# Kernel tuning notes

Measured on AMD Instinct MI355X. Metric: run time of the kernel, lower is better.

Reference implementation:

```python
import jax, jax.numpy as jnp
import numpy as np

K = 1024          # num_embeddings
D = 256           # embedding_dim
COMMITMENT = 0.25


def setup_inputs() -> dict:
    key = jax.random.key(0)
    k1, k2, k3 = jax.random.split(key, 3)
    return {
        "inputs": jax.random.normal(k1, (64, 2048, D), dtype=jnp.float32),
        "pre_w": jax.random.normal(k2, (D, D), dtype=jnp.float32) / jnp.sqrt(jnp.float32(D)),
        "pre_b": jnp.zeros((D,), dtype=jnp.float32),
        "emb": jax.random.uniform(k3, (K, D), dtype=jnp.float32, minval=-1.0, maxval=1.0),
    }


def reference(inputs, pre_w, pre_b, emb):
    # flatten to tokens [N, D] and apply pre_linear
    flat = inputs.reshape(-1, D)
    f = flat @ pre_w.T + pre_b                       # [N, D]
    # squared euclidean distances to codebook: ||f||^2 + ||e||^2 - 2 f e^T
    distances = (jnp.sum(f * f, axis=1, keepdims=True)
                 + jnp.sum(emb * emb, axis=1)
                 - 2.0 * (f @ emb.T))                # [N, K]
    idx = jnp.argmin(distances, axis=1)              # [N]
    encodings = jax.nn.one_hot(idx, K, dtype=inputs.dtype)  # [N, K]
    # quantized = encodings @ emb  ==  gather rows of codebook
    quantized = emb[idx].reshape(inputs.shape)       # [B, S, D]
    # commitment loss (quantized detached)
    e_latent_loss = jnp.mean((jax.lax.stop_gradient(quantized) - inputs) ** 2)
    loss = COMMITMENT * e_latent_loss
    # straight-through estimator
    quantized_st = inputs + jax.lax.stop_gradient(quantized - inputs)
    avg_probs = jnp.mean(encodings, axis=0)          # [K]
    perplexity = jnp.exp(-jnp.sum(avg_probs * jnp.log(avg_probs + 1e-10)))
    return loss, quantized_st, perplexity, encodings
```

## Files before the change

### kernel.cpp

```cpp
#include <hip/hip_runtime.h>
#include <math.h>

#define NTOK 131072
#define DDIM 256
#define KCB  1024

static constexpr size_t O_Q = 1;
static constexpr size_t O_P = 1 + (size_t)NTOK * DDIM;
static constexpr size_t O_E = O_P + 1;
static constexpr size_t SCRATCH_F_OFF = O_E + 2;
static constexpr size_t SCRATCH_FHI   = SCRATCH_F_OFF + (size_t)NTOK * DDIM;
static constexpr size_t SCRATCH_FLO   = SCRATCH_FHI + (size_t)NTOK * DDIM / 2;
static constexpr size_t SCRATCH_EHI   = SCRATCH_FLO + (size_t)NTOK * DDIM / 2;
static constexpr size_t SCRATCH_ELO   = SCRATCH_EHI + (size_t)KCB * DDIM / 2;
static constexpr size_t SCRATCH_FLG   = SCRATCH_ELO + (size_t)KCB * DDIM / 2;

static constexpr size_t WS_IDX   = 0;
static constexpr size_t WS_EN    = (size_t)NTOK * 4;
static constexpr size_t WS_CNT   = WS_EN + (size_t)KCB * 4;
static constexpr size_t WS_ACC   = WS_CNT + (size_t)KCB * 4;
static constexpr size_t WS_FLAGN = WS_ACC + 8;

#define TS 128
#define KC 32
#define LDSROW 36

#define EPS_GAP 0.0625f

typedef short bf16x8 __attribute__((ext_vector_type(8)));
typedef float f32x4  __attribute__((ext_vector_type(4)));
typedef unsigned short us4v __attribute__((ext_vector_type(4)));

__device__ __forceinline__ unsigned short f2bf(float x) {
    unsigned u = __float_as_uint(x);
    return (unsigned short)((u + 0x7FFFu + ((u >> 16) & 1u)) >> 16);
}
__device__ __forceinline__ float bf2f(unsigned short h) {
    return __uint_as_float(((unsigned)h) << 16);
}

__global__ __launch_bounds__(64) void k_enorm(const float* __restrict__ emb,
                                              float* __restrict__ enorm,
                                              unsigned short* __restrict__ ehi,
                                              unsigned short* __restrict__ elo) {
    int k = blockIdx.x;
    float4 v = reinterpret_cast<const float4*>(emb)[(size_t)k * 64 + threadIdx.x];
    float s = v.x * v.x + v.y * v.y + v.z * v.z + v.w * v.w;

    float xs[4] = {v.x, v.y, v.z, v.w};
    us4v hv, lv;
#pragma unroll
    for (int i = 0; i < 4; ++i) {
        unsigned short h = f2bf(xs[i]);
        hv[i] = h;
        lv[i] = f2bf(xs[i] - bf2f(h));
    }
    *reinterpret_cast<us4v*>(ehi + (size_t)k * DDIM + threadIdx.x * 4) = hv;
    *reinterpret_cast<us4v*>(elo + (size_t)k * DDIM + threadIdx.x * 4) = lv;

    for (int off = 32; off >= 1; off >>= 1) s += __shfl_down(s, off, 64);
    if (threadIdx.x == 0) enorm[k] = s;
}

__device__ __forceinline__ void tile_fma(const float* __restrict__ sA,
                                         const float* __restrict__ sB,
                                         int tx, int ty,
                                         float acc[8][8]) {
#pragma unroll 1
    for (int is = 0; is < 8; ++is) {
        float4 bv[8];
#pragma unroll
        for (int c = 0; c < 8; ++c)
            bv[c] = *reinterpret_cast<const float4*>(&sB[(tx + 16 * c) * LDSROW + is * 4]);
#pragma unroll
        for (int j = 0; j < 8; ++j) {
            float4 a = *reinterpret_cast<const float4*>(&sA[(ty + 16 * j) * LDSROW + is * 4]);
#pragma unroll
            for (int c = 0; c < 8; ++c)
                acc[j][c] += a.x * bv[c].x + a.y * bv[c].y + a.z * bv[c].z + a.w * bv[c].w;
        }
    }
}

__device__ __forceinline__ void stage_tiles(const float4* __restrict__ a4, size_t a_row0,
                                            const float4* __restrict__ b4, size_t b_row0,
                                            int kc, int tid,
                                            float* __restrict__ sA, float* __restrict__ sB) {
#pragma unroll
    for (int l0 = 0; l0 < 4; ++l0) {
        int l = l0 * 256 + tid;
        int row = l >> 3, i4 = l & 7;
        *reinterpret_cast<float4*>(&sA[row * LDSROW + i4 * 4]) =
            a4[(a_row0 + row) * 64 + kc * 8 + i4];
        *reinterpret_cast<float4*>(&sB[row * LDSROW + i4 * 4]) =
            b4[(b_row0 + row) * 64 + kc * 8 + i4];
    }
}

__global__ __launch_bounds__(256, 2) void k_gemm1(const float* __restrict__ x,
                                                  const float* __restrict__ w,
                                                  const float* __restrict__ b,
                                                  float* __restrict__ f,
                                                  unsigned short* __restrict__ fhi,
                                                  unsigned short* __restrict__ flo) {
    __shared__ float sA[TS * LDSROW];
    __shared__ float sB[TS * LDSROW];
    const int tid = threadIdx.x;
    const int tx = tid & 15, ty = tid >> 4;
    const int tb = blockIdx.x * TS;
    const int db = blockIdx.y * TS;

    float acc[8][8];
#pragma unroll
    for (int j = 0; j < 8; ++j)
#pragma unroll
        for (int c = 0; c < 8; ++c) acc[j][c] = 0.f;

    const float4* x4 = reinterpret_cast<const float4*>(x);
    const float4* w4 = reinterpret_cast<const float4*>(w);

#pragma unroll 1
    for (int kc = 0; kc < DDIM / KC; ++kc) {
        __syncthreads();
        stage_tiles(x4, tb, w4, db, kc, tid, sA, sB);
        __syncthreads();
        tile_fma(sA, sB, tx, ty, acc);
    }

    float bias[8];
#pragma unroll
    for (int c = 0; c < 8; ++c) bias[c] = b[db + tx + 16 * c];
#pragma unroll
    for (int j = 0; j < 8; ++j) {
        size_t rowo = (size_t)(tb + ty + 16 * j) * DDIM + db;
#pragma unroll
        for (int c = 0; c < 8; ++c) {
            float v = acc[j][c] + bias[c];
            int col = tx + 16 * c;
            f[rowo + col] = v;
            unsigned short h = f2bf(v);
            fhi[rowo + col] = h;
            flo[rowo + col] = f2bf(v - bf2f(h));
        }
    }
}

__global__ __launch_bounds__(256, 2) void k_argmin_mfma(
        const unsigned short* __restrict__ fhi, const unsigned short* __restrict__ flo,
        const unsigned short* __restrict__ ehi, const unsigned short* __restrict__ elo,
        const float* __restrict__ enorm,
        int* __restrict__ idx, int* __restrict__ flaglist, unsigned* __restrict__ flagn) {
    __shared__ bf16x8 sB[1024];
    const int tid  = threadIdx.x;
    const int lane = tid & 63;
    const int wv   = tid >> 6;
    const int row  = lane & 15;
    const int kg   = lane >> 4;
    const int tok0 = blockIdx.x * 128 + wv * 32;

    bf16x8 ah[2][8], al[2][8];
#pragma unroll
    for (int m = 0; m < 2; ++m)
#pragma unroll
        for (int kk = 0; kk < 8; ++kk) {
            size_t off = (size_t)(tok0 + m * 16 + row) * DDIM + kk * 32 + kg * 8;
            ah[m][kk] = *reinterpret_cast<const bf16x8*>(fhi + off);
            al[m][kk] = *reinterpret_cast<const bf16x8*>(flo + off);
        }

    float bd1[2][4], bd2[2][4];
    int   bk1[2][4];
#pragma unroll
    for (int m = 0; m < 2; ++m)
#pragma unroll
        for (int r = 0; r < 4; ++r) { bd1[m][r] = 3.4e38f; bd2[m][r] = 3.4e38f; bk1[m][r] = 0; }

    const int sxr = row & 7;

#pragma unroll 1
    for (int nt = 0; nt < KCB / 16; ++nt) {
        bf16x8 st[4];
#pragma unroll
        for (int i = 0; i < 4; ++i) {
            int c = i * 256 + tid;
            int code = (c >> 5) & 15, ch = c & 31;
            const unsigned short* src = (c < 512) ? ehi : elo;
            st[i] = *reinterpret_cast<const bf16x8*>(src + (size_t)(nt * 16 + code) * DDIM + ch * 8);
        }
        __syncthreads();
#pragma unroll
        for (int i = 0; i < 4; ++i) {
            int c = i * 256 + tid;
            int code = (c >> 5) & 15, ch = c & 31;
            sB[((c < 512) ? 0 : 512) + code * 32 + (ch ^ (code & 7))] = st[i];
        }
        __syncthreads();

        f32x4 acc0a = {0.f, 0.f, 0.f, 0.f}, acc0b = {0.f, 0.f, 0.f, 0.f};
        f32x4 acc1a = {0.f, 0.f, 0.f, 0.f}, acc1b = {0.f, 0.f, 0.f, 0.f};
#pragma unroll
        for (int kk = 0; kk < 8; ++kk) {
            int slot = row * 32 + (((kk * 4) + kg) ^ sxr);
            bf16x8 bh = sB[slot];
            bf16x8 bl = sB[512 + slot];
            acc0a = __builtin_amdgcn_mfma_f32_16x16x32_bf16(ah[0][kk], bh, acc0a, 0, 0, 0);
            acc1a = __builtin_amdgcn_mfma_f32_16x16x32_bf16(ah[1][kk], bh, acc1a, 0, 0, 0);
            acc0b = __builtin_amdgcn_mfma_f32_16x16x32_bf16(al[0][kk], bh, acc0b, 0, 0, 0);
            acc1b = __builtin_amdgcn_mfma_f32_16x16x32_bf16(al[1][kk], bh, acc1b, 0, 0, 0);
            acc0b = __builtin_amdgcn_mfma_f32_16x16x32_bf16(ah[0][kk], bl, acc0b, 0, 0, 0);
            acc1b = __builtin_amdgcn_mfma_f32_16x16x32_bf16(ah[1][kk], bl, acc1b, 0, 0, 0);
        }

        int code = nt * 16 + row;
        float en = enorm[code];
#pragma unroll
        for (int r = 0; r < 4; ++r) {
            float d0 = en - 2.f * (acc0a[r] + acc0b[r]);
            float d1 = en - 2.f * (acc1a[r] + acc1b[r]);
            if (d0 < bd1[0][r]) { bd2[0][r] = bd1[0][r]; bd1[0][r] = d0; bk1[0][r] = code; }
            else if (d0 < bd2[0][r]) bd2[0][r] = d0;
            if (d1 < bd1[1][r]) { bd2[1][r] = bd1[1][r]; bd1[1][r] = d1; bk1[1][r] = code; }
            else if (d1 < bd2[1][r]) bd2[1][r] = d1;
        }
    }

#pragma unroll
    for (int m = 0; m < 2; ++m)
#pragma unroll
        for (int r = 0; r < 4; ++r) {
            float v1 = bd1[m][r], v2 = bd2[m][r];
            int k1 = bk1[m][r];
#pragma unroll
            for (int msk = 1; msk < 16; msk <<= 1) {
                float o1 = __shfl_xor(v1, msk, 16);
                float o2 = __shfl_xor(v2, msk, 16);
                int   ok = __shfl_xor(k1, msk, 16);
                if (o1 < v1 || (o1 == v1 && ok < k1)) { v2 = fminf(v1, o2); v1 = o1; k1 = ok; }
                else                                  { v2 = fminf(v2, o1); }
            }
            if (row == 0) {
                int t = tok0 + m * 16 + kg * 4 + r;
                idx[t] = k1;
                if (v2 - v1 < EPS_GAP) {
                    unsigned p = atomicAdd(flagn, 1u);
                    flaglist[p] = t;
                }
            }
        }
}

__global__ __launch_bounds__(256) void k_rescore(const float* __restrict__ f,
                                                 const float* __restrict__ emb,
                                                 const float* __restrict__ enorm,
                                                 const int* __restrict__ flaglist,
                                                 const unsigned* __restrict__ flagn,
                                                 int* __restrict__ idx) {
    __shared__ float sf[DDIM];
    __shared__ float swd[4];
    __shared__ int   swk[4];
    const int tid = threadIdx.x;
    const unsigned n = *flagn;
    for (unsigned ii = blockIdx.x; ii < n; ii += gridDim.x) {
        const int t = flaglist[ii];
        __syncthreads();
        sf[tid] = f[(size_t)t * DDIM + tid];
        __syncthreads();
        float bd = 3.4e38f;
        int   bk = 0;
#pragma unroll 1
        for (int j = 0; j < 4; ++j) {
            int k = j * 256 + tid;
            const float4* er = reinterpret_cast<const float4*>(emb + (size_t)k * DDIM);
            float dot = 0.f;
#pragma unroll 8
            for (int q = 0; q < 64; ++q) {
                float4 ev = er[q];
                float4 fv = *reinterpret_cast<const float4*>(&sf[q * 4]);
                dot += ev.x * fv.x + ev.y * fv.y + ev.z * fv.z + ev.w * fv.w;
            }
            float d = enorm[k] - 2.f * dot;
            if (d < bd || (d == bd && k < bk)) { bd = d; bk = k; }
        }
        for (int m = 1; m < 64; m <<= 1) {
            float od = __shfl_xor(bd, m, 64);
            int   ok = __shfl_xor(bk, m, 64);
            if (od < bd || (od == bd && ok < bk)) { bd = od; bk = ok; }
        }
        if ((tid & 63) == 0) { swd[tid >> 6] = bd; swk[tid >> 6] = bk; }
        __syncthreads();
        if (tid == 0) {
            for (int w2 = 1; w2 < 4; ++w2)
                if (swd[w2] < bd || (swd[w2] == bd && swk[w2] < bk)) { bd = swd[w2]; bk = swk[w2]; }
            idx[t] = bk;
        }
    }
}

__global__ __launch_bounds__(256) void k_epilogue(const float* __restrict__ x,
                                                  const float* __restrict__ emb,
                                                  const int* __restrict__ idx,
                                                  float* __restrict__ out,
                                                  unsigned* __restrict__ counts,
                                                  double* __restrict__ lossacc) {
    const int tid = threadIdx.x;
    const int tb = blockIdx.x * 64;
    const float4* x4 = reinterpret_cast<const float4*>(x);
    const float4* e4 = reinterpret_cast<const float4*>(emb);
    float local = 0.f;
#pragma unroll
    for (int it = 0; it < 16; ++it) {
        int l = it * 256 + tid;
        int tok = l >> 6, q = l & 63;
        int t = tb + tok;
        int id = idx[t];
        if (q == 0) atomicAdd(&counts[id], 1u);
        float4 xv = x4[(size_t)t * 64 + q];
        float4 ev = e4[(size_t)id * 64 + q];
        size_t o = O_Q + (size_t)t * DDIM + (size_t)q * 4;
        out[o] = ev.x; out[o + 1] = ev.y; out[o + 2] = ev.z; out[o + 3] = ev.w;
        float dx = ev.x - xv.x, dy = ev.y - xv.y, dz = ev.z - xv.z, dw = ev.w - xv.w;
        local += dx * dx + dy * dy + dz * dz + dw * dw;
    }
    for (int off = 32; off >= 1; off >>= 1) local += __shfl_down(local, off, 64);
    __shared__ float wsum[4];
    if ((tid & 63) == 0) wsum[tid >> 6] = local;
    __syncthreads();
    if (tid == 0)
        atomicAdd(lossacc, (double)(wsum[0] + wsum[1] + wsum[2] + wsum[3]));
}

__global__ __launch_bounds__(256) void k_scatter(const int* __restrict__ idx,
                                                 float* __restrict__ out) {
    int t = blockIdx.x * 256 + threadIdx.x;
    out[O_E + (size_t)t * KCB + idx[t]] = 1.0f;
}

__global__ __launch_bounds__(1024) void k_final(const unsigned* __restrict__ counts,
                                                const double* __restrict__ lossacc,
                                                float* __restrict__ out) {
    int tid = threadIdx.x;
    double p = (double)counts[tid] / (double)NTOK;
    double term = p * log(p + 1e-10);
    for (int off = 32; off >= 1; off >>= 1) term += __shfl_down(term, off, 64);
    __shared__ double sw[16];
    if ((tid & 63) == 0) sw[tid >> 6] = term;
    __syncthreads();
    if (tid == 0) {
        double s = 0.0;
        for (int i = 0; i < 16; ++i) s += sw[i];
        out[O_P] = (float)exp(-s);
        out[0]   = (float)(0.25 * lossacc[0] / ((double)NTOK * (double)DDIM));
    }
}

extern "C" void kernel_launch(void* const* d_in, const int* in_sizes, int n_in,
                              void* d_out, int out_size, void* d_ws, size_t ws_size,
                              hipStream_t stream) {
    const float* x   = (const float*)d_in[0];
    const float* w   = (const float*)d_in[1];
    const float* b   = (const float*)d_in[2];
    const float* emb = (const float*)d_in[3];
    float* out = (float*)d_out;

    int*      idx    = (int*)((char*)d_ws + WS_IDX);
    float*    enorm  = (float*)((char*)d_ws + WS_EN);
    unsigned* counts = (unsigned*)((char*)d_ws + WS_CNT);
    double*   acc    = (double*)((char*)d_ws + WS_ACC);
    unsigned* flagn  = (unsigned*)((char*)d_ws + WS_FLAGN);

    float*          scratchF = out + SCRATCH_F_OFF;
    unsigned short* fhi      = (unsigned short*)(out + SCRATCH_FHI);
    unsigned short* flo      = (unsigned short*)(out + SCRATCH_FLO);
    unsigned short* ehi      = (unsigned short*)(out + SCRATCH_EHI);
    unsigned short* elo      = (unsigned short*)(out + SCRATCH_ELO);
    int*            flaglist = (int*)(out + SCRATCH_FLG);

    hipMemsetAsync((char*)d_ws + WS_CNT, 0, (size_t)KCB * 4 + 16, stream);

    k_enorm      <<<KCB,                        64,  0, stream>>>(emb, enorm, ehi, elo);
    k_gemm1      <<<dim3(NTOK / TS, DDIM / TS), 256, 0, stream>>>(x, w, b, scratchF, fhi, flo);
    k_argmin_mfma<<<NTOK / 128,                 256, 0, stream>>>(fhi, flo, ehi, elo, enorm,
                                                                 idx, flaglist, flagn);
    k_rescore    <<<128,                        256, 0, stream>>>(scratchF, emb, enorm,
                                                                 flaglist, flagn, idx);
    k_epilogue   <<<NTOK / 64,                  256, 0, stream>>>(x, emb, idx, out, counts, acc);

    hipMemsetAsync(out + O_E, 0, (size_t)NTOK * KCB * 4, stream);
    k_scatter<<<NTOK / 256, 256, 0, stream>>>(idx, out);
    k_final  <<<1,          1024, 0, stream>>>(counts, acc, out);
}
```

Before: 1.677 ms.

## Drop fp32 feature scratch, fuse one-hot write into epilogue, prefetch GEMM tiles

Removes the fp32 f scratch buffer: gemm1 writes only bf16 hi/lo splits, and rescore recomputes f for flagged tokens from x, w and bias. The memset and scatter for the one-hot encodings are replaced by a single pass in the epilogue that writes each full row directly. The next tiles are register-prefetched in gemm1 and in the argmin codebook staging so global loads overlap compute. These changes cut DRAM traffic and kernel launches, at the cost of extra register pressure and redundant matvec work in rescore.

```diff
diff --git a/kernel.cpp b/kernel.cpp
--- a/kernel.cpp
+++ b/kernel.cpp
@@ -8,12 +8,11 @@
 static constexpr size_t O_Q = 1;
 static constexpr size_t O_P = 1 + (size_t)NTOK * DDIM;
 static constexpr size_t O_E = O_P + 1;
-static constexpr size_t SCRATCH_F_OFF = O_E + 2;
-static constexpr size_t SCRATCH_FHI   = SCRATCH_F_OFF + (size_t)NTOK * DDIM;
-static constexpr size_t SCRATCH_FLO   = SCRATCH_FHI + (size_t)NTOK * DDIM / 2;
-static constexpr size_t SCRATCH_EHI   = SCRATCH_FLO + (size_t)NTOK * DDIM / 2;
-static constexpr size_t SCRATCH_ELO   = SCRATCH_EHI + (size_t)KCB * DDIM / 2;
-static constexpr size_t SCRATCH_FLG   = SCRATCH_ELO + (size_t)KCB * DDIM / 2;
+static constexpr size_t SCRATCH_FHI = O_E + 2;
+static constexpr size_t SCRATCH_FLO = SCRATCH_FHI + (size_t)NTOK * DDIM / 2;
+static constexpr size_t SCRATCH_EHI = SCRATCH_FLO + (size_t)NTOK * DDIM / 2;
+static constexpr size_t SCRATCH_ELO = SCRATCH_EHI + (size_t)KCB * DDIM / 2;
+static constexpr size_t SCRATCH_FLG = SCRATCH_ELO + (size_t)KCB * DDIM / 2;
 
 static constexpr size_t WS_IDX   = 0;
 static constexpr size_t WS_EN    = (size_t)NTOK * 4;
@@ -82,25 +81,9 @@
     }
 }
 
-__device__ __forceinline__ void stage_tiles(const float4* __restrict__ a4, size_t a_row0,
-                                            const float4* __restrict__ b4, size_t b_row0,
-                                            int kc, int tid,
-                                            float* __restrict__ sA, float* __restrict__ sB) {
-#pragma unroll
-    for (int l0 = 0; l0 < 4; ++l0) {
-        int l = l0 * 256 + tid;
-        int row = l >> 3, i4 = l & 7;
-        *reinterpret_cast<float4*>(&sA[row * LDSROW + i4 * 4]) =
-            a4[(a_row0 + row) * 64 + kc * 8 + i4];
-        *reinterpret_cast<float4*>(&sB[row * LDSROW + i4 * 4]) =
-            b4[(b_row0 + row) * 64 + kc * 8 + i4];
-    }
-}
-
 __global__ __launch_bounds__(256, 2) void k_gemm1(const float* __restrict__ x,
                                                   const float* __restrict__ w,
                                                   const float* __restrict__ b,
-                                                  float* __restrict__ f,
                                                   unsigned short* __restrict__ fhi,
                                                   unsigned short* __restrict__ flo) {
     __shared__ float sA[TS * LDSROW];
@@ -119,11 +102,33 @@
     const float4* x4 = reinterpret_cast<const float4*>(x);
     const float4* w4 = reinterpret_cast<const float4*>(w);
 
+    const int pr = tid >> 3, pi = tid & 7;
+    float4 pa[4], pb[4];
+#pragma unroll
+    for (int l0 = 0; l0 < 4; ++l0) {
+        int row = l0 * 32 + pr;
+        pa[l0] = x4[(size_t)(tb + row) * 64 + pi];
+        pb[l0] = w4[(size_t)(db + row) * 64 + pi];
+    }
+
 #pragma unroll 1
     for (int kc = 0; kc < DDIM / KC; ++kc) {
         __syncthreads();
-        stage_tiles(x4, tb, w4, db, kc, tid, sA, sB);
-        __syncthreads();
+#pragma unroll
+        for (int l0 = 0; l0 < 4; ++l0) {
+            int row = l0 * 32 + pr;
+            *reinterpret_cast<float4*>(&sA[row * LDSROW + pi * 4]) = pa[l0];
+            *reinterpret_cast<float4*>(&sB[row * LDSROW + pi * 4]) = pb[l0];
+        }
+        __syncthreads();
+        if (kc < DDIM / KC - 1) {
+#pragma unroll
+            for (int l0 = 0; l0 < 4; ++l0) {
+                int row = l0 * 32 + pr;
+                pa[l0] = x4[(size_t)(tb + row) * 64 + (kc + 1) * 8 + pi];
+                pb[l0] = w4[(size_t)(db + row) * 64 + (kc + 1) * 8 + pi];
+            }
+        }
         tile_fma(sA, sB, tx, ty, acc);
     }
 
@@ -137,7 +142,6 @@
         for (int c = 0; c < 8; ++c) {
             float v = acc[j][c] + bias[c];
             int col = tx + 16 * c;
-            f[rowo + col] = v;
             unsigned short h = f2bf(v);
             fhi[rowo + col] = h;
             flo[rowo + col] = f2bf(v - bf2f(h));
@@ -176,17 +180,20 @@
         for (int r = 0; r < 4; ++r) { bd1[m][r] = 3.4e38f; bd2[m][r] = 3.4e38f; bk1[m][r] = 0; }
 
     const int sxr = row & 7;
+    const int pcode = (tid >> 5) & 15, pch = tid & 31;
+    const bool plo = tid >= 512 / 1;
+
+    bf16x8 st[4];
+#pragma unroll
+    for (int i = 0; i < 4; ++i) {
+        int c = i * 256 + tid;
+        int code = (c >> 5) & 15, ch = c & 31;
+        const unsigned short* src = (c < 512) ? ehi : elo;
+        st[i] = *reinterpret_cast<const bf16x8*>(src + (size_t)code * DDIM + ch * 8);
+    }
 
 #pragma unroll 1
     for (int nt = 0; nt < KCB / 16; ++nt) {
-        bf16x8 st[4];
-#pragma unroll
-        for (int i = 0; i < 4; ++i) {
-            int c = i * 256 + tid;
-            int code = (c >> 5) & 15, ch = c & 31;
-            const unsigned short* src = (c < 512) ? ehi : elo;
-            st[i] = *reinterpret_cast<const bf16x8*>(src + (size_t)(nt * 16 + code) * DDIM + ch * 8);
-        }
         __syncthreads();
 #pragma unroll
         for (int i = 0; i < 4; ++i) {
@@ -195,6 +202,16 @@
             sB[((c < 512) ? 0 : 512) + code * 32 + (ch ^ (code & 7))] = st[i];
         }
         __syncthreads();
+        if (nt < KCB / 16 - 1) {
+#pragma unroll
+            for (int i = 0; i < 4; ++i) {
+                int c = i * 256 + tid;
+                int code = (c >> 5) & 15, ch = c & 31;
+                const unsigned short* src = (c < 512) ? ehi : elo;
+                st[i] = *reinterpret_cast<const bf16x8*>(
+                    src + (size_t)((nt + 1) * 16 + code) * DDIM + ch * 8);
+            }
+        }
 
         f32x4 acc0a = {0.f, 0.f, 0.f, 0.f}, acc0b = {0.f, 0.f, 0.f, 0.f};
         f32x4 acc1a = {0.f, 0.f, 0.f, 0.f}, acc1b = {0.f, 0.f, 0.f, 0.f};
@@ -249,12 +266,15 @@
         }
 }
 
-__global__ __launch_bounds__(256) void k_rescore(const float* __restrict__ f,
+__global__ __launch_bounds__(256) void k_rescore(const float* __restrict__ x,
+                                                 const float* __restrict__ w,
+                                                 const float* __restrict__ bias,
                                                  const float* __restrict__ emb,
                                                  const float* __restrict__ enorm,
                                                  const int* __restrict__ flaglist,
                                                  const unsigned* __restrict__ flagn,
                                                  int* __restrict__ idx) {
+    __shared__ float sx[DDIM];
     __shared__ float sf[DDIM];
     __shared__ float swd[4];
     __shared__ int   swk[4];
@@ -263,7 +283,17 @@
     for (unsigned ii = blockIdx.x; ii < n; ii += gridDim.x) {
         const int t = flaglist[ii];
         __syncthreads();
-        sf[tid] = f[(size_t)t * DDIM + tid];
+        sx[tid] = x[(size_t)t * DDIM + tid];
+        __syncthreads();
+        const float4* wr = reinterpret_cast<const float4*>(w + (size_t)tid * DDIM);
+        float fd = bias[tid];
+#pragma unroll 8
+        for (int q = 0; q < 64; ++q) {
+            float4 wv = wr[q];
+            float4 xv = *reinterpret_cast<const float4*>(&sx[q * 4]);
+            fd += wv.x * xv.x + wv.y * xv.y + wv.z * xv.z + wv.w * xv.w;
+        }
+        sf[tid] = fd;
         __syncthreads();
         float bd = 3.4e38f;
         int   bk = 0;
@@ -296,14 +326,19 @@
     }
 }
 
-__global__ __launch_bounds__(256) void k_epilogue(const float* __restrict__ x,
-                                                  const float* __restrict__ emb,
-                                                  const int* __restrict__ idx,
-                                                  float* __restrict__ out,
-                                                  unsigned* __restrict__ counts,
-                                                  double* __restrict__ lossacc) {
+__global__ __launch_bounds__(256) void k_out(const float* __restrict__ x,
+                                             const float* __restrict__ emb,
+                                             const int* __restrict__ idx,
+                                             float* __restrict__ out,
+                                             unsigned* __restrict__ counts,
+                                             double* __restrict__ lossacc) {
     const int tid = threadIdx.x;
     const int tb = blockIdx.x * 64;
+    __shared__ int   sidx[64];
+    __shared__ float wsum[4];
+    if (tid < 64) sidx[tid] = idx[tb + tid];
+    __syncthreads();
+
     const float4* x4 = reinterpret_cast<const float4*>(x);
     const float4* e4 = reinterpret_cast<const float4*>(emb);
     float local = 0.f;
@@ -312,7 +347,7 @@
         int l = it * 256 + tid;
         int tok = l >> 6, q = l & 63;
         int t = tb + tok;
-        int id = idx[t];
+        int id = sidx[tok];
         if (q == 0) atomicAdd(&counts[id], 1u);
         float4 xv = x4[(size_t)t * 64 + q];
         float4 ev = e4[(size_t)id * 64 + q];
@@ -322,17 +357,24 @@
         local += dx * dx + dy * dy + dz * dz + dw * dw;
     }
     for (int off = 32; off >= 1; off >>= 1) local += __shfl_down(local, off, 64);
-    __shared__ float wsum[4];
     if ((tid & 63) == 0) wsum[tid >> 6] = local;
     __syncthreads();
     if (tid == 0)
         atomicAdd(lossacc, (double)(wsum[0] + wsum[1] + wsum[2] + wsum[3]));
-}
-
-__global__ __launch_bounds__(256) void k_scatter(const int* __restrict__ idx,
-                                                 float* __restrict__ out) {
-    int t = blockIdx.x * 256 + threadIdx.x;
-    out[O_E + (size_t)t * KCB + idx[t]] = 1.0f;
+
+#pragma unroll 1
+    for (int r = 0; r < 64; ++r) {
+        int id = sidx[r];
+        float* rb = out + O_E + (size_t)(tb + r) * KCB;
+        int hot = id >> 1, sub = id & 1;
+#pragma unroll
+        for (int i = 0; i < 2; ++i) {
+            int q2 = i * 256 + tid;
+            float2 v = make_float2(0.f, 0.f);
+            if (q2 == hot) { if (sub) v.y = 1.f; else v.x = 1.f; }
+            *reinterpret_cast<float2*>(rb + (size_t)q2 * 2) = v;
+        }
+    }
 }
 
 __global__ __launch_bounds__(1024) void k_final(const unsigned* __restrict__ counts,
@@ -368,7 +410,6 @@
     double*   acc    = (double*)((char*)d_ws + WS_ACC);
     unsigned* flagn  = (unsigned*)((char*)d_ws + WS_FLAGN);
 
-    float*          scratchF = out + SCRATCH_F_OFF;
     unsigned short* fhi      = (unsigned short*)(out + SCRATCH_FHI);
     unsigned short* flo      = (unsigned short*)(out + SCRATCH_FLO);
     unsigned short* ehi      = (unsigned short*)(out + SCRATCH_EHI);
@@ -378,14 +419,11 @@
     hipMemsetAsync((char*)d_ws + WS_CNT, 0, (size_t)KCB * 4 + 16, stream);
 
     k_enorm      <<<KCB,                        64,  0, stream>>>(emb, enorm, ehi, elo);
-    k_gemm1      <<<dim3(NTOK / TS, DDIM / TS), 256, 0, stream>>>(x, w, b, scratchF, fhi, flo);
+    k_gemm1      <<<dim3(NTOK / TS, DDIM / TS), 256, 0, stream>>>(x, w, b, fhi, flo);
     k_argmin_mfma<<<NTOK / 128,                 256, 0, stream>>>(fhi, flo, ehi, elo, enorm,
                                                                  idx, flaglist, flagn);
-    k_rescore    <<<128,                        256, 0, stream>>>(scratchF, emb, enorm,
+    k_rescore    <<<128,                        256, 0, stream>>>(x, w, b, emb, enorm,
                                                                  flaglist, flagn, idx);
-    k_epilogue   <<<NTOK / 64,                  256, 0, stream>>>(x, emb, idx, out, counts, acc);
-
-    hipMemsetAsync(out + O_E, 0, (size_t)NTOK * KCB * 4, stream);
-    k_scatter<<<NTOK / 256, 256, 0, stream>>>(idx, out);
-    k_final  <<<1,          1024, 0, stream>>>(counts, acc, out);
-}
+    k_out        <<<NTOK / 64,                  256, 0, stream>>>(x, emb, idx, out, counts, acc);
+    k_final      <<<1,                          1024, 0, stream>>>(counts, acc, out);
+}
```

Measured after the change: 1.788 ms. 6.6% more time.
